# Optimization experiments

Hardware: AMD Instinct MI355X
Metric: run time of the kernel (lower is better)

## Reference

```python
import jax, jax.numpy as jnp
import numpy as np

TAU = 1.0       # softmax_temp
SOS_IDX = 1
EOS_IDX = 2
MAX_LEN = 20    # total message length incl. SOS/EOS -> 18 decode steps


def setup_inputs() -> dict:
    key = jax.random.key(0)
    ks = jax.random.split(key, 12)
    B, E, H, V, F = 512, 256, 512, 4096, 512
    T = MAX_LEN - 2
    s = lambda k, shape, sc: jax.random.normal(k, shape, jnp.float32) * sc
    return {
        "proto_a": s(ks[0], (B, F), 1.0),
        "proto_b": s(ks[1], (B, F), 1.0),
        "W_init": s(ks[2], (H, 2 * F), (2 * F) ** -0.5),
        "b_init": jnp.zeros((H,), jnp.float32),
        "W_ih": s(ks[3], (3 * H, E), E ** -0.5),
        "W_hh": s(ks[4], (3 * H, H), H ** -0.5),
        "b_ih": jnp.zeros((3 * H,), jnp.float32),
        "b_hh": jnp.zeros((3 * H,), jnp.float32),
        "W_out": s(ks[5], (V, H), H ** -0.5),
        "b_out": jnp.zeros((V,), jnp.float32),
        "emb": s(ks[6], (V, E), 1.0),
        # uniforms in (0,1) turned into Gumbel noise inside reference
        "u_gumbel": jax.random.uniform(ks[7], (T, B, V), jnp.float32, 1e-6, 1.0 - 1e-6),
    }


def reference(proto_a, proto_b, W_init, b_init, W_ih, W_hh, b_ih, b_hh,
              W_out, b_out, emb, u_gumbel):
    B = proto_a.shape[0]
    V = W_out.shape[0]
    # init_h(cat(prototypes, 1)) -> h0 [B, H]
    h0 = jnp.concatenate([proto_a, proto_b], axis=1) @ W_init.T + b_init
    sos = jnp.zeros((B, V), h0.dtype).at[:, SOS_IDX].set(1.0)
    eos = jnp.zeros((B, V), h0.dtype).at[:, EOS_IDX].set(1.0)
    x0 = sos @ emb  # [B, E]
    g = -jnp.log(-jnp.log(u_gumbel))  # Gumbel(0,1) noise, [T, B, V]

    def step(carry, gt):
        h, x = carry  # h [B,H], x [B,E]
        # PyTorch single-step GRU cell
        gi = x @ W_ih.T + b_ih
        gh = h @ W_hh.T + b_hh
        ir, iz, inn = jnp.split(gi, 3, axis=-1)
        hr, hz, hn = jnp.split(gh, 3, axis=-1)
        r = jax.nn.sigmoid(ir + hr)
        z = jax.nn.sigmoid(iz + hz)
        n = jnp.tanh(inn + r * hn)
        h_new = (1.0 - z) * n + z * h
        logits = h_new @ W_out.T + b_out  # [B, V]
        # gumbel_softmax(tau, hard=False) then straight-through hard one-hot
        y = jax.nn.softmax((logits + gt) / TAU, axis=-1)
        hard = jax.nn.one_hot(jnp.argmax(y, axis=-1), V, dtype=y.dtype)
        onehot = hard - jax.lax.stop_gradient(y) + y
        return (h_new, onehot @ emb), onehot

    _, toks = jax.lax.scan(step, (h0, x0), g)  # toks [T, B, V]
    lang = jnp.concatenate([sos[:, None], jnp.swapaxes(toks, 0, 1), eos[:, None]], axis=1)
    return lang  # [B, MAX_LEN, V]
```

## Files before the change

kernel.cpp:

```cpp
#include <hip/hip_runtime.h>
#include <hip/hip_bf16.h>
#include <math.h>

#define B_ 512
#define E_ 256
#define H_ 512
#define V_ 4096
#define T_ 18
#define L_ 20
#define MARGIN_ 0.04f
#define CCAP_ 64

typedef __attribute__((ext_vector_type(8))) short bf16x8;
typedef __attribute__((ext_vector_type(4))) float f32x4;

__global__ __launch_bounds__(256) void kprep32(const float* __restrict__ pa,
                                               const float* __restrict__ pb,
                                               const float* __restrict__ Wout,
                                               float* __restrict__ cat,
                                               __hip_bfloat16* __restrict__ WB) {
  int idx = blockIdx.x * 256 + threadIdx.x;
  if (idx < 131072) {
    int e0 = idx * 4;
    int b = e0 >> 10, k = e0 & 1023;
    float4 v = (k < 512) ? *reinterpret_cast<const float4*>(pa + (size_t)b * 512 + k)
                         : *reinterpret_cast<const float4*>(pb + (size_t)b * 512 + (k - 512));
    *reinterpret_cast<float4*>(cat + e0) = v;
  } else {
    int e0 = (idx - 131072) * 4;
    float4 w = *reinterpret_cast<const float4*>(Wout + e0);
    __hip_bfloat16 b0 = __float2bfloat16(w.x), b1 = __float2bfloat16(w.y);
    __hip_bfloat16 b2 = __float2bfloat16(w.z), b3 = __float2bfloat16(w.w);
    ushort4 o;
    o.x = *reinterpret_cast<unsigned short*>(&b0);
    o.y = *reinterpret_cast<unsigned short*>(&b1);
    o.z = *reinterpret_cast<unsigned short*>(&b2);
    o.w = *reinterpret_cast<unsigned short*>(&b3);
    *reinterpret_cast<ushort4*>(WB + e0) = o;
  }
}

__global__ __launch_bounds__(256) void sgemm128(const float* __restrict__ A,
                                                const float* __restrict__ W,
                                                float* __restrict__ P,
                                                int N, int lda, int kPer) {
  __shared__ float As[16][132];
  __shared__ float Bs[16][132];
  const int tid = threadIdx.x;
  const int tx = tid & 15, ty = tid >> 4;
  const int bn = blockIdx.x * 128, bm = blockIdx.y * 128;
  const int k0 = blockIdx.z * kPer;
  const size_t pOff = (size_t)blockIdx.z * (size_t)gridDim.y * 128 * N;
  const int r1 = tid >> 2;
  const int kq = (tid & 3) * 4;

  float acc[8][8] = {};
  for (int kb = 0; kb < kPer; kb += 16) {
    const float* Ap = A + (size_t)(bm + r1) * lda + k0 + kb + kq;
    const float* Wp = W + (size_t)(bn + r1) * lda + k0 + kb + kq;
    float4 a1 = *reinterpret_cast<const float4*>(Ap);
    float4 a2 = *reinterpret_cast<const float4*>(Ap + (size_t)64 * lda);
    float4 b1 = *reinterpret_cast<const float4*>(Wp);
    float4 b2 = *reinterpret_cast<const float4*>(Wp + (size_t)64 * lda);
    As[kq + 0][r1] = a1.x; As[kq + 1][r1] = a1.y;
    As[kq + 2][r1] = a1.z; As[kq + 3][r1] = a1.w;
    As[kq + 0][r1 + 64] = a2.x; As[kq + 1][r1 + 64] = a2.y;
    As[kq + 2][r1 + 64] = a2.z; As[kq + 3][r1 + 64] = a2.w;
    Bs[kq + 0][r1] = b1.x; Bs[kq + 1][r1] = b1.y;
    Bs[kq + 2][r1] = b1.z; Bs[kq + 3][r1] = b1.w;
    Bs[kq + 0][r1 + 64] = b2.x; Bs[kq + 1][r1 + 64] = b2.y;
    Bs[kq + 2][r1 + 64] = b2.z; Bs[kq + 3][r1 + 64] = b2.w;
    __syncthreads();
#pragma unroll
    for (int kk = 0; kk < 16; ++kk) {
      float a[8], b[8];
#pragma unroll
      for (int i = 0; i < 8; ++i) a[i] = As[kk][ty * 8 + i];
#pragma unroll
      for (int j = 0; j < 8; ++j) b[j] = Bs[kk][tx * 8 + j];
#pragma unroll
      for (int i = 0; i < 8; ++i)
#pragma unroll
        for (int j = 0; j < 8; ++j) acc[i][j] = fmaf(a[i], b[j], acc[i][j]);
    }
    __syncthreads();
  }
#pragma unroll
  for (int i = 0; i < 8; ++i) {
    size_t r = (size_t)(bm + ty * 8 + i);
    float4 v0 = make_float4(acc[i][0], acc[i][1], acc[i][2], acc[i][3]);
    float4 v1 = make_float4(acc[i][4], acc[i][5], acc[i][6], acc[i][7]);
    float4* dst = reinterpret_cast<float4*>(P + pOff + r * N + bn + tx * 8);
    dst[0] = v0;
    dst[1] = v1;
  }
}

__global__ __launch_bounds__(256) void reduceH0(const float* __restrict__ parts,
                                                const float* __restrict__ binit,
                                                float* __restrict__ h,
                                                __hip_bfloat16* __restrict__ hB) {
  int i = blockIdx.x * 256 + threadIdx.x;
  double s = (double)binit[i & 511];
#pragma unroll
  for (int c = 0; c < 8; ++c) s += (double)parts[(size_t)c * 262144 + i];
  float f = (float)s;
  h[i] = f;
  hB[i] = __float2bfloat16(f);
}

__device__ __forceinline__ void gh_gemm_body(const float* __restrict__ h,
                                             const float* __restrict__ Whh,
                                             float* __restrict__ ghP,
                                             int gid, int tid, char* smemRaw) {
  float (*As)[132] = reinterpret_cast<float(*)[132]>(smemRaw);
  float (*Bs)[132] = reinterpret_cast<float(*)[132]>(smemRaw + 8448);
  const int tx = tid & 15, ty = tid >> 4;
  const int bx = gid % 12, by = (gid / 12) & 3, bz = gid / 48;
  const int bn = bx * 128, bm = by * 128;
  const int k0 = bz * 64;
  const size_t pOff = (size_t)bz * 786432;
  const int r1 = tid >> 2, kq = (tid & 3) * 4;
  float acc[8][8] = {};
  for (int kb = 0; kb < 64; kb += 16) {
    const float* Ap = h   + (size_t)(bm + r1) * H_ + k0 + kb + kq;
    const float* Wp = Whh + (size_t)(bn + r1) * H_ + k0 + kb + kq;
    float4 a1 = *reinterpret_cast<const float4*>(Ap);
    float4 a2 = *reinterpret_cast<const float4*>(Ap + (size_t)64 * H_);
    float4 b1 = *reinterpret_cast<const float4*>(Wp);
    float4 b2 = *reinterpret_cast<const float4*>(Wp + (size_t)64 * H_);
    As[kq + 0][r1] = a1.x; As[kq + 1][r1] = a1.y;
    As[kq + 2][r1] = a1.z; As[kq + 3][r1] = a1.w;
    As[kq + 0][r1 + 64] = a2.x; As[kq + 1][r1 + 64] = a2.y;
    As[kq + 2][r1 + 64] = a2.z; As[kq + 3][r1 + 64] = a2.w;
    Bs[kq + 0][r1] = b1.x; Bs[kq + 1][r1] = b1.y;
    Bs[kq + 2][r1] = b1.z; Bs[kq + 3][r1] = b1.w;
    Bs[kq + 0][r1 + 64] = b2.x; Bs[kq + 1][r1 + 64] = b2.y;
    Bs[kq + 2][r1 + 64] = b2.z; Bs[kq + 3][r1 + 64] = b2.w;
    __syncthreads();
#pragma unroll
    for (int kk = 0; kk < 16; ++kk) {
      float a[8], b[8];
#pragma unroll
      for (int i = 0; i < 8; ++i) a[i] = As[kk][ty * 8 + i];
#pragma unroll
      for (int j = 0; j < 8; ++j) b[j] = Bs[kk][tx * 8 + j];
#pragma unroll
      for (int i = 0; i < 8; ++i)
#pragma unroll
        for (int j = 0; j < 8; ++j) acc[i][j] = fmaf(a[i], b[j], acc[i][j]);
    }
    __syncthreads();
  }
#pragma unroll
  for (int i = 0; i < 8; ++i) {
    size_t r = (size_t)(bm + ty * 8 + i);
    float4 v0 = make_float4(acc[i][0], acc[i][1], acc[i][2], acc[i][3]);
    float4 v1 = make_float4(acc[i][4], acc[i][5], acc[i][6], acc[i][7]);
    float4* dst = reinterpret_cast<float4*>(ghP + pOff + r * 1536 + bn + tx * 8);
    dst[0] = v0;
    dst[1] = v1;
  }
}

__device__ __forceinline__ void screen_body(const __hip_bfloat16* __restrict__ hB,
                                            const __hip_bfloat16* __restrict__ WoutB,
                                            float* __restrict__ loP,
                                            int bid, int tid) {
  const int wave = tid >> 6, lane = tid & 63;
  const int bx = bid & 63, by = bid >> 6;
  const int bm = by * 64 + wave * 16;
  const int bn = bx * 64;
  const int rA = lane & 15, g = lane >> 4;
  const __hip_bfloat16* ha = hB + (size_t)(bm + rA) * H_ + g * 8;
  const __hip_bfloat16* wb = WoutB + (size_t)(bn + rA) * H_ + g * 8;
  f32x4 acc[4] = {};
  for (int k0 = 0; k0 < H_; k0 += 32) {
    bf16x8 a = *reinterpret_cast<const bf16x8*>(ha + k0);
#pragma unroll
    for (int j = 0; j < 4; ++j) {
      bf16x8 b = *reinterpret_cast<const bf16x8*>(wb + (size_t)j * 16 * H_ + k0);
      acc[j] = __builtin_amdgcn_mfma_f32_16x16x32_bf16(a, b, acc[j], 0, 0, 0);
    }
  }
#pragma unroll
  for (int j = 0; j < 4; ++j)
#pragma unroll
    for (int r = 0; r < 4; ++r)
      loP[(size_t)(bm + g * 4 + r) * V_ + bn + j * 16 + rA] = acc[j][r];
}

__device__ __forceinline__ void gates_body(const float* __restrict__ ghP,
                                           const float* __restrict__ giP,
                                           const float* __restrict__ bih,
                                           const float* __restrict__ bhh,
                                           int tok, float* __restrict__ h,
                                           __hip_bfloat16* __restrict__ hB,
                                           int bid, int tid) {
  const float* g0 = giP + (size_t)tok * 1536;
  size_t base = (size_t)bid * 1536;
#pragma unroll
  for (int c = 0; c < 2; ++c) {
    int j = c * 256 + tid;
    int idx = bid * 512 + j;
    double gr = (double)bhh[j], gz = (double)bhh[512 + j], gn = (double)bhh[1024 + j];
#pragma unroll
    for (int s = 0; s < 8; ++s) {
      const float* p = ghP + (size_t)s * 786432 + base;
      gr += (double)p[j]; gz += (double)p[512 + j]; gn += (double)p[1024 + j];
    }
    float ir  = g0[j]        + bih[j];
    float iz  = g0[512 + j]  + bih[512 + j];
    float inn = g0[1024 + j] + bih[1024 + j];
    float r = 1.f / (1.f + expf(-(ir + (float)gr)));
    float z = 1.f / (1.f + expf(-(iz + (float)gz)));
    float n = tanhf(inn + r * (float)gn);
    float hn = (1.f - z) * n + z * h[idx];
    h[idx] = hn;
    hB[idx] = __float2bfloat16(hn);
  }
}

__device__ __forceinline__ int pick_body(const float* __restrict__ loP,
                                         const float* __restrict__ h,
                                         const float* __restrict__ Wout,
                                         const float* __restrict__ bout,
                                         const float* __restrict__ ub,
                                         int bid, int tid, char* smemRaw) {
  double* sd    = reinterpret_cast<double*>(smemRaw);
  int*    pre   = reinterpret_cast<int*>(smemRaw + 2048);
  int*    candV = reinterpret_cast<int*>(smemRaw + 3072);
  float*  swv   = reinterpret_cast<float*>(smemRaw + 3328);
  int*    swi   = reinterpret_cast<int*>(smemRaw + 3344);
  int*    sct   = reinterpret_cast<int*>(smemRaw + 3360);
  double* bestS = reinterpret_cast<double*>(smemRaw + 3376);
  int*    bestV = reinterpret_cast<int*>(smemRaw + 3384);
  const int lane = tid & 63, wv = tid >> 6;
  const float* l0 = loP + (size_t)bid * V_;
  float sloc[16];
  float best = -1e30f; int bi = 0x7fffffff;
#pragma unroll
  for (int i = 0; i < 16; ++i) {
    int v = tid + 256 * i;
    float s = l0[v] + bout[v] - logf(-logf(ub[v]));
    sloc[i] = s;
    if (s > best) { best = s; bi = v; }
  }
#pragma unroll
  for (int off = 1; off < 64; off <<= 1) {
    float ov = __shfl_xor(best, off, 64);
    int   oi = __shfl_xor(bi,  off, 64);
    if (ov > best || (ov == best && oi < bi)) { best = ov; bi = oi; }
  }
  if (lane == 0) { swv[wv] = best; swi[wv] = bi; }
  __syncthreads();
  float smax = swv[0]; int amax = swi[0];
#pragma unroll
  for (int w = 1; w < 4; ++w) {
    float ov = swv[w]; int oi = swi[w];
    if (ov > smax || (ov == smax && oi < amax)) { smax = ov; amax = oi; }
  }
  int c = 0;
#pragma unroll
  for (int i = 0; i < 16; ++i) if (sloc[i] >= smax - MARGIN_) ++c;
  int csum = c;
#pragma unroll
  for (int off = 1; off < 64; off <<= 1) csum += __shfl_xor(csum, off, 64);
  if (lane == 0) sct[wv] = csum;
  __syncthreads();
  int tot = sct[0] + sct[1] + sct[2] + sct[3];

  int tok;
  if (tot == 1) {
    tok = amax;
  } else if (tot <= CCAP_) {
    int lv[16];
    int cc = 0;
#pragma unroll
    for (int i = 0; i < 16; ++i)
      if (sloc[i] >= smax - MARGIN_) { if (cc < 16) lv[cc] = tid + 256 * i; ++cc; }
    pre[tid] = cc;
    __syncthreads();
    for (int off = 1; off < 256; off <<= 1) {
      int vv = (tid >= off) ? pre[tid - off] : 0;
      __syncthreads();
      pre[tid] += vv;
      __syncthreads();
    }
    int base = pre[tid] - cc;
    for (int q = 0; q < cc; ++q) candV[base + q] = lv[q];
    if (tid == 0) { *bestS = -1e300; *bestV = 0x7fffffff; }
    __syncthreads();
    const float* hb = h + (size_t)bid * H_;
    for (int ci = 0; ci < tot; ++ci) {
      int v = candV[ci];
      const float* wr = Wout + (size_t)v * H_;
      double p = (double)hb[tid] * (double)wr[tid]
               + (double)hb[tid + 256] * (double)wr[tid + 256];
#pragma unroll
      for (int off = 1; off < 64; off <<= 1) p += __shfl_xor(p, off, 64);
      if (lane == 0) sd[wv] = p;
      __syncthreads();
      if (tid == 0) {
        double s = sd[0] + sd[1] + sd[2] + sd[3]
                 + (double)bout[v] - log(-log((double)ub[v]));
        if (s > *bestS || (s == *bestS && v < *bestV)) { *bestS = s; *bestV = v; }
      }
      __syncthreads();
    }
    tok = *bestV;
  } else {
    const float* hb = h + (size_t)bid * H_;
    double dbest = -1e300; int dbi = 0x7fffffff;
    for (int i = 0; i < 16; ++i) {
      int v = tid + 256 * i;
      const float* wr = Wout + (size_t)v * H_;
      double dot = 0.0;
      for (int k = 0; k < H_; ++k) dot = fma((double)hb[k], (double)wr[k], dot);
      double s = dot + (double)bout[v] - log(-log((double)ub[v]));
      if (s > dbest) { dbest = s; dbi = v; }
    }
#pragma unroll
    for (int off = 1; off < 64; off <<= 1) {
      double od = __shfl_xor(dbest, off, 64);
      int    oi = __shfl_xor(dbi,  off, 64);
      if (od > dbest || (od == dbest && oi < dbi)) { dbest = od; dbi = oi; }
    }
    if (lane == 0) { sd[wv] = dbest; pre[wv] = dbi; }
    __syncthreads();
    double bs = sd[0]; int bv = pre[0];
#pragma unroll
    for (int w = 1; w < 4; ++w) {
      if (sd[w] > bs || (sd[w] == bs && pre[w] < bv)) { bs = sd[w]; bv = pre[w]; }
    }
    tok = bv;
  }
  return tok;
}

__global__ __launch_bounds__(256) void gates_init(const float* __restrict__ ghP,
                                                  const float* __restrict__ giP,
                                                  const float* __restrict__ bih,
                                                  const float* __restrict__ bhh,
                                                  float* __restrict__ h,
                                                  __hip_bfloat16* __restrict__ hB) {
  gates_body(ghP, giP, bih, bhh, 1, h, hB, blockIdx.x, threadIdx.x);
}

__global__ __launch_bounds__(256) void fusedA(const float* __restrict__ h,
                                              const float* __restrict__ Whh,
                                              const __hip_bfloat16* __restrict__ hB,
                                              const __hip_bfloat16* __restrict__ WoutB,
                                              float* __restrict__ ghP,
                                              float* __restrict__ loP,
                                              int doGemm) {
  __shared__ __align__(16) char smemRaw[16896];
  const int bid = blockIdx.x, tid = threadIdx.x;
  if (bid < 384) {
    if (doGemm) gh_gemm_body(h, Whh, ghP, bid, tid, smemRaw);
  } else {
    screen_body(hB, WoutB, loP, bid - 384, tid);
  }
}

__global__ __launch_bounds__(256) void fusedB(const float* __restrict__ loP,
                                              float* __restrict__ h,
                                              const float* __restrict__ Wout,
                                              const float* __restrict__ bout,
                                              const float* __restrict__ u,
                                              const float* __restrict__ ghP,
                                              const float* __restrict__ giP,
                                              const float* __restrict__ bih,
                                              const float* __restrict__ bhh,
                                              __hip_bfloat16* __restrict__ hB,
                                              int* __restrict__ toks,
                                              int t, int doGates) {
  __shared__ __align__(16) char smemRaw[5440];
  const int bid = blockIdx.x, tid = threadIdx.x;
  const int j0 = tid, j1 = 256 + tid;
  double gr0 = (double)bhh[j0], gz0 = (double)bhh[512 + j0], gn0 = (double)bhh[1024 + j0];
  double gr1 = (double)bhh[j1], gz1 = (double)bhh[512 + j1], gn1 = (double)bhh[1024 + j1];
  if (doGates) {
    size_t base = (size_t)bid * 1536;
#pragma unroll
    for (int s = 0; s < 8; ++s) {
      const float* p = ghP + (size_t)s * 786432 + base;
      gr0 += (double)p[j0]; gz0 += (double)p[512 + j0]; gn0 += (double)p[1024 + j0];
      gr1 += (double)p[j1]; gz1 += (double)p[512 + j1]; gn1 += (double)p[1024 + j1];
    }
  }
  const float* ub = u + (size_t)bid * V_;
  int tok = pick_body(loP, h, Wout, bout, ub, bid, tid, smemRaw);
  if (tid == 0) toks[t * B_ + bid] = tok;
  if (doGates) {
    const float* g0 = giP + (size_t)tok * 1536;
    {
      int idx = bid * 512 + j0;
      float ir  = g0[j0]        + bih[j0];
      float iz  = g0[512 + j0]  + bih[512 + j0];
      float inn = g0[1024 + j0] + bih[1024 + j0];
      float r = 1.f / (1.f + expf(-(ir + (float)gr0)));
      float z = 1.f / (1.f + expf(-(iz + (float)gz0)));
      float n = tanhf(inn + r * (float)gn0);
      float hn = (1.f - z) * n + z * h[idx];
      h[idx] = hn;
      hB[idx] = __float2bfloat16(hn);
    }
    {
      int idx = bid * 512 + j1;
      float ir  = g0[j1]        + bih[j1];
      float iz  = g0[512 + j1]  + bih[512 + j1];
      float inn = g0[1024 + j1] + bih[1024 + j1];
      float r = 1.f / (1.f + expf(-(ir + (float)gr1)));
      float z = 1.f / (1.f + expf(-(iz + (float)gz1)));
      float n = tanhf(inn + r * (float)gn1);
      float hn = (1.f - z) * n + z * h[idx];
      h[idx] = hn;
      hB[idx] = __float2bfloat16(hn);
    }
  }
}

__global__ __launch_bounds__(256) void kfinal32(float* __restrict__ out,
                                                const int* __restrict__ toks) {
  size_t c = (size_t)blockIdx.x * 256 + threadIdx.x;
  size_t e0 = c * 4;
  int v0 = (int)(e0 & (size_t)(V_ - 1));
  size_t row = e0 >> 12;
  int p = (int)(row % L_);
  int b = (int)(row / L_);
  int tok;
  if (p == 0)           tok = 1;
  else if (p == L_ - 1) tok = 2;
  else                  tok = toks[(p - 1) * B_ + b];
  float4 val = make_float4(0.f, 0.f, 0.f, 0.f);
  int d = tok - v0;
  if (d >= 0 && d < 4) {
    if (d == 0) val.x = 1.f; else if (d == 1) val.y = 1.f;
    else if (d == 2) val.z = 1.f; else val.w = 1.f;
  }
  reinterpret_cast<float4*>(out)[c] = val;
}

__global__ void kmark_ws(float* out) {
  if (threadIdx.x == 0) out[0] = 16.0f;
}
__global__ void kmark_resolver(float* out) {
  if (threadIdx.x == 0) out[2] = 11.0f;
}

extern "C" void kernel_launch(void* const* d_in, const int* in_sizes, int n_in,
                              void* d_out, int out_size, void* d_ws, size_t ws_size,
                              hipStream_t stream) {
  static const int EXPECT[12] = {262144, 262144, 524288, 512, 393216, 786432,
                                 1536, 1536, 2097152, 4096, 1048576, 37748736};
  const float* R[12];
  bool resolved = (n_in == 12);
  if (resolved) {
    bool used[12] = {};
    for (int i = 0; i < 12; ++i) {
      int f = -1;
      for (int j = 0; j < 12; ++j)
        if (!used[j] && in_sizes[j] == EXPECT[i]) { f = j; break; }
      if (f < 0) { resolved = false; break; }
      used[f] = true;
      R[i] = (const float*)d_in[f];
    }
  }
  if (!resolved)
    for (int i = 0; i < 12 && i < n_in; ++i) R[i] = (const float*)d_in[i];

  const float *pa = R[0], *pb = R[1], *Winit = R[2], *binit = R[3],
              *Wih = R[4], *Whh = R[5], *bih = R[6], *bhh = R[7],
              *Wout = R[8], *bout = R[9], *emb = R[10], *ug = R[11];
  float* out = (float*)d_out;

  const size_t TOK_BYTES = (size_t)T_ * B_ * sizeof(int);
  if (ws_size < TOK_BYTES) { kmark_ws<<<1, 64, 0, stream>>>(out); return; }
  int* toks = (int*)d_ws;

  const size_t SC_FLOATS = 16121856;
  float* sc;
  if (ws_size >= 40960 + SC_FLOATS * sizeof(float)) {
    sc = (float*)((char*)d_ws + 40960);
  } else {
    sc = (float*)d_out;
  }
  float* h    = sc;
  float* giP  = sc + 262144;
  float* ghP  = sc + 6553600;
  float* loP  = sc + 12845056;
  __hip_bfloat16* hB    = (__hip_bfloat16*)(sc + 14942208);
  __hip_bfloat16* WoutB = (__hip_bfloat16*)(sc + 15073280);
  float* cat  = ghP;
  float* h0P  = ghP + 524288;

  kprep32<<<2560, 256, 0, stream>>>(pa, pb, Wout, cat, WoutB);
  sgemm128<<<dim3(4, 4, 8), 256, 0, stream>>>(cat, Winit, h0P, 512, 1024, 128);
  reduceH0<<<1024, 256, 0, stream>>>(h0P, binit, h, hB);
  sgemm128<<<dim3(12, 32, 1), 256, 0, stream>>>(emb, Wih, giP, 1536, 256, 256);
  sgemm128<<<dim3(12, 4, 8), 256, 0, stream>>>(h, Whh, ghP, 1536, 512, 64);
  gates_init<<<512, 256, 0, stream>>>(ghP, giP, bih, bhh, h, hB);

  for (int t = 0; t < T_; ++t) {
    const float* uslice = ug + (size_t)t * B_ * V_;
    int notLast = (t < T_ - 1) ? 1 : 0;
    fusedA<<<896, 256, 0, stream>>>(h, Whh, hB, WoutB, ghP, loP, notLast);
    fusedB<<<512, 256, 0, stream>>>(loP, h, Wout, bout, uslice, ghP, giP,
                                    bih, bhh, hB, toks, t, notLast);
  }

  kfinal32<<<40960, 256, 0, stream>>>(out, toks);
  if (!resolved) kmark_resolver<<<1, 64, 0, stream>>>(out);
}
```

Before: 945.5 us.

## Fuse gumbel noise and bias into screen GEMM epilogue with per-block max pruning

Moves the bias add and Gumbel noise computation into the bf16 logit screening GEMM epilogue and records a per-64-column block maximum for each row. The pick kernel then reduces the 64 block maxima and scans only the blocks within the margin, instead of reading the full 4096-wide row plus noise on every step. This cuts the work and memory traffic in the serial pick stage. In exchange, the GEMM epilogue does the log computations and writes an extra bMax buffer, and the exact-rescore path now reloads the full row.

```diff
diff --git a/kernel.cpp b/kernel.cpp
--- a/kernel.cpp
+++ b/kernel.cpp
@@ -165,7 +165,10 @@
 
 __device__ __forceinline__ void screen_body(const __hip_bfloat16* __restrict__ hB,
                                             const __hip_bfloat16* __restrict__ WoutB,
+                                            const float* __restrict__ bout,
+                                            const float* __restrict__ u,
                                             float* __restrict__ loP,
+                                            float* __restrict__ bMax,
                                             int bid, int tid) {
   const int wave = tid >> 6, lane = tid & 63;
   const int bx = bid & 63, by = bid >> 6;
@@ -183,102 +186,97 @@
       acc[j] = __builtin_amdgcn_mfma_f32_16x16x32_bf16(a, b, acc[j], 0, 0, 0);
     }
   }
-#pragma unroll
-  for (int j = 0; j < 4; ++j)
-#pragma unroll
-    for (int r = 0; r < 4; ++r)
-      loP[(size_t)(bm + g * 4 + r) * V_ + bn + j * 16 + rA] = acc[j][r];
-}
-
-__device__ __forceinline__ void gates_body(const float* __restrict__ ghP,
-                                           const float* __restrict__ giP,
-                                           const float* __restrict__ bih,
-                                           const float* __restrict__ bhh,
-                                           int tok, float* __restrict__ h,
-                                           __hip_bfloat16* __restrict__ hB,
-                                           int bid, int tid) {
-  const float* g0 = giP + (size_t)tok * 1536;
-  size_t base = (size_t)bid * 1536;
-#pragma unroll
-  for (int c = 0; c < 2; ++c) {
-    int j = c * 256 + tid;
-    int idx = bid * 512 + j;
-    double gr = (double)bhh[j], gz = (double)bhh[512 + j], gn = (double)bhh[1024 + j];
-#pragma unroll
-    for (int s = 0; s < 8; ++s) {
-      const float* p = ghP + (size_t)s * 786432 + base;
-      gr += (double)p[j]; gz += (double)p[512 + j]; gn += (double)p[1024 + j];
-    }
-    float ir  = g0[j]        + bih[j];
-    float iz  = g0[512 + j]  + bih[512 + j];
-    float inn = g0[1024 + j] + bih[1024 + j];
-    float r = 1.f / (1.f + expf(-(ir + (float)gr)));
-    float z = 1.f / (1.f + expf(-(iz + (float)gz)));
-    float n = tanhf(inn + r * (float)gn);
-    float hn = (1.f - z) * n + z * h[idx];
-    h[idx] = hn;
-    hB[idx] = __float2bfloat16(hn);
+  float bj[4];
+#pragma unroll
+  for (int j = 0; j < 4; ++j) bj[j] = bout[bn + j * 16 + rA];
+#pragma unroll
+  for (int r = 0; r < 4; ++r) {
+    int row = bm + g * 4 + r;
+    const float* ur = u + (size_t)row * V_ + bn;
+    float m = -1e30f;
+#pragma unroll
+    for (int j = 0; j < 4; ++j) {
+      float s = acc[j][r] + bj[j] - logf(-logf(ur[j * 16 + rA]));
+      loP[(size_t)row * V_ + bn + j * 16 + rA] = s;
+      m = fmaxf(m, s);
+    }
+#pragma unroll
+    for (int off = 1; off < 16; off <<= 1) m = fmaxf(m, __shfl_xor(m, off, 64));
+    if (rA == 0) bMax[(size_t)row * 64 + bx] = m;
   }
 }
 
 __device__ __forceinline__ int pick_body(const float* __restrict__ loP,
+                                         const float* __restrict__ bMax,
                                          const float* __restrict__ h,
                                          const float* __restrict__ Wout,
                                          const float* __restrict__ bout,
                                          const float* __restrict__ ub,
                                          int bid, int tid, char* smemRaw) {
   double* sd    = reinterpret_cast<double*>(smemRaw);
-  int*    pre   = reinterpret_cast<int*>(smemRaw + 2048);
-  int*    candV = reinterpret_cast<int*>(smemRaw + 3072);
-  float*  swv   = reinterpret_cast<float*>(smemRaw + 3328);
-  int*    swi   = reinterpret_cast<int*>(smemRaw + 3344);
-  int*    sct   = reinterpret_cast<int*>(smemRaw + 3360);
-  double* bestS = reinterpret_cast<double*>(smemRaw + 3376);
-  int*    bestV = reinterpret_cast<int*>(smemRaw + 3384);
+  double* bestS = reinterpret_cast<double*>(smemRaw + 32);
+  int*    bestV = reinterpret_cast<int*>(smemRaw + 40);
+  int*    sNcb  = reinterpret_cast<int*>(smemRaw + 44);
+  float*  sRow  = reinterpret_cast<float*>(smemRaw + 48);
+  float*  swv   = reinterpret_cast<float*>(smemRaw + 56);
+  int*    swi   = reinterpret_cast<int*>(smemRaw + 72);
+  int*    sct   = reinterpret_cast<int*>(smemRaw + 88);
+  int*    candB = reinterpret_cast<int*>(smemRaw + 104);
+  int*    candV = reinterpret_cast<int*>(smemRaw + 360);
+  int*    pre   = reinterpret_cast<int*>(smemRaw + 640);
   const int lane = tid & 63, wv = tid >> 6;
   const float* l0 = loP + (size_t)bid * V_;
-  float sloc[16];
-  float best = -1e30f; int bi = 0x7fffffff;
-#pragma unroll
-  for (int i = 0; i < 16; ++i) {
-    int v = tid + 256 * i;
-    float s = l0[v] + bout[v] - logf(-logf(ub[v]));
-    sloc[i] = s;
-    if (s > best) { best = s; bi = v; }
+
+  if (wv == 0) {
+    float bm = bMax[(size_t)bid * 64 + lane];
+    float m = bm;
+#pragma unroll
+    for (int off = 1; off < 64; off <<= 1) m = fmaxf(m, __shfl_xor(m, off, 64));
+    unsigned long long mask = __ballot(bm >= m - MARGIN_);
+    int pos = __popcll(mask & ((1ull << lane) - 1ull));
+    if (bm >= m - MARGIN_) candB[pos] = lane;
+    if (lane == 0) { *sRow = m; *sNcb = __popcll(mask); }
+  }
+  __syncthreads();
+  float smax = *sRow;
+  int ncb = *sNcb;
+
+  float best = -1e30f; int bi = 0x7fffffff; int cnt = 0;
+  for (int e = tid; e < ncb * 64; e += 256) {
+    int v = candB[e >> 6] * 64 + (e & 63);
+    float s = l0[v];
+    if (s > best || (s == best && v < bi)) { best = s; bi = v; }
+    if (s >= smax - MARGIN_) ++cnt;
   }
 #pragma unroll
   for (int off = 1; off < 64; off <<= 1) {
     float ov = __shfl_xor(best, off, 64);
     int   oi = __shfl_xor(bi,  off, 64);
     if (ov > best || (ov == best && oi < bi)) { best = ov; bi = oi; }
-  }
-  if (lane == 0) { swv[wv] = best; swi[wv] = bi; }
+    cnt += __shfl_xor(cnt, off, 64);
+  }
+  if (lane == 0) { swv[wv] = best; swi[wv] = bi; sct[wv] = cnt; }
   __syncthreads();
-  float smax = swv[0]; int amax = swi[0];
+  float gmax = swv[0]; int amax = swi[0];
 #pragma unroll
   for (int w = 1; w < 4; ++w) {
     float ov = swv[w]; int oi = swi[w];
-    if (ov > smax || (ov == smax && oi < amax)) { smax = ov; amax = oi; }
-  }
-  int c = 0;
-#pragma unroll
-  for (int i = 0; i < 16; ++i) if (sloc[i] >= smax - MARGIN_) ++c;
-  int csum = c;
-#pragma unroll
-  for (int off = 1; off < 64; off <<= 1) csum += __shfl_xor(csum, off, 64);
-  if (lane == 0) sct[wv] = csum;
-  __syncthreads();
+    if (ov > gmax || (ov == gmax && oi < amax)) { gmax = ov; amax = oi; }
+  }
   int tot = sct[0] + sct[1] + sct[2] + sct[3];
 
   int tok;
   if (tot == 1) {
     tok = amax;
   } else if (tot <= CCAP_) {
+    float sloc[16];
+#pragma unroll
+    for (int i = 0; i < 16; ++i) sloc[i] = l0[tid + 256 * i];
     int lv[16];
     int cc = 0;
 #pragma unroll
     for (int i = 0; i < 16; ++i)
-      if (sloc[i] >= smax - MARGIN_) { if (cc < 16) lv[cc] = tid + 256 * i; ++cc; }
+      if (sloc[i] >= gmax - MARGIN_) { if (cc < 16) lv[cc] = tid + 256 * i; ++cc; }
     pre[tid] = cc;
     __syncthreads();
     for (int off = 1; off < 256; off <<= 1) {
@@ -344,26 +342,52 @@
                                                   const float* __restrict__ bhh,
                                                   float* __restrict__ h,
                                                   __hip_bfloat16* __restrict__ hB) {
-  gates_body(ghP, giP, bih, bhh, 1, h, hB, blockIdx.x, threadIdx.x);
+  const int bid = blockIdx.x, tid = threadIdx.x;
+  const float* g0 = giP + (size_t)1 * 1536;
+  size_t base = (size_t)bid * 1536;
+#pragma unroll
+  for (int c = 0; c < 2; ++c) {
+    int j = c * 256 + tid;
+    int idx = bid * 512 + j;
+    double gr = (double)bhh[j], gz = (double)bhh[512 + j], gn = (double)bhh[1024 + j];
+#pragma unroll
+    for (int s = 0; s < 8; ++s) {
+      const float* p = ghP + (size_t)s * 786432 + base;
+      gr += (double)p[j]; gz += (double)p[512 + j]; gn += (double)p[1024 + j];
+    }
+    float ir  = g0[j]        + bih[j];
+    float iz  = g0[512 + j]  + bih[512 + j];
+    float inn = g0[1024 + j] + bih[1024 + j];
+    float r = 1.f / (1.f + expf(-(ir + (float)gr)));
+    float z = 1.f / (1.f + expf(-(iz + (float)gz)));
+    float n = tanhf(inn + r * (float)gn);
+    float hn = (1.f - z) * n + z * h[idx];
+    h[idx] = hn;
+    hB[idx] = __float2bfloat16(hn);
+  }
 }
 
 __global__ __launch_bounds__(256) void fusedA(const float* __restrict__ h,
                                               const float* __restrict__ Whh,
                                               const __hip_bfloat16* __restrict__ hB,
                                               const __hip_bfloat16* __restrict__ WoutB,
+                                              const float* __restrict__ bout,
+                                              const float* __restrict__ u,
                                               float* __restrict__ ghP,
                                               float* __restrict__ loP,
+                                              float* __restrict__ bMax,
                                               int doGemm) {
   __shared__ __align__(16) char smemRaw[16896];
   const int bid = blockIdx.x, tid = threadIdx.x;
   if (bid < 384) {
     if (doGemm) gh_gemm_body(h, Whh, ghP, bid, tid, smemRaw);
   } else {
-    screen_body(hB, WoutB, loP, bid - 384, tid);
+    screen_body(hB, WoutB, bout, u, loP, bMax, bid - 384, tid);
   }
 }
 
 __global__ __launch_bounds__(256) void fusedB(const float* __restrict__ loP,
+                                              const float* __restrict__ bMax,
                                               float* __restrict__ h,
                                               const float* __restrict__ Wout,
                                               const float* __restrict__ bout,
@@ -375,7 +399,7 @@
                                               __hip_bfloat16* __restrict__ hB,
                                               int* __restrict__ toks,
                                               int t, int doGates) {
-  __shared__ __align__(16) char smemRaw[5440];
+  __shared__ __align__(16) char smemRaw[2048];
   const int bid = blockIdx.x, tid = threadIdx.x;
   const int j0 = tid, j1 = 256 + tid;
   double gr0 = (double)bhh[j0], gz0 = (double)bhh[512 + j0], gn0 = (double)bhh[1024 + j0];
@@ -390,7 +414,7 @@
     }
   }
   const float* ub = u + (size_t)bid * V_;
-  int tok = pick_body(loP, h, Wout, bout, ub, bid, tid, smemRaw);
+  int tok = pick_body(loP, bMax, h, Wout, bout, ub, bid, tid, smemRaw);
   if (tid == 0) toks[t * B_ + bid] = tok;
   if (doGates) {
     const float* g0 = giP + (size_t)tok * 1536;
@@ -479,7 +503,7 @@
   if (ws_size < TOK_BYTES) { kmark_ws<<<1, 64, 0, stream>>>(out); return; }
   int* toks = (int*)d_ws;
 
-  const size_t SC_FLOATS = 16121856;
+  const size_t SC_FLOATS = 16154624;
   float* sc;
   if (ws_size >= 40960 + SC_FLOATS * sizeof(float)) {
     sc = (float*)((char*)d_ws + 40960);
@@ -492,6 +516,7 @@
   float* loP  = sc + 12845056;
   __hip_bfloat16* hB    = (__hip_bfloat16*)(sc + 14942208);
   __hip_bfloat16* WoutB = (__hip_bfloat16*)(sc + 15073280);
+  float* bMax = sc + 16121856;
   float* cat  = ghP;
   float* h0P  = ghP + 524288;
 
@@ -505,8 +530,9 @@
   for (int t = 0; t < T_; ++t) {
     const float* uslice = ug + (size_t)t * B_ * V_;
     int notLast = (t < T_ - 1) ? 1 : 0;
-    fusedA<<<896, 256, 0, stream>>>(h, Whh, hB, WoutB, ghP, loP, notLast);
-    fusedB<<<512, 256, 0, stream>>>(loP, h, Wout, bout, uslice, ghP, giP,
+    fusedA<<<896, 256, 0, stream>>>(h, Whh, hB, WoutB, bout, uslice,
+                                    ghP, loP, bMax, notLast);
+    fusedB<<<512, 256, 0, stream>>>(loP, bMax, h, Wout, bout, uslice, ghP, giP,
                                     bih, bhh, hB, toks, t, notLast);
   }
 
```

Measured after the change: 1.016 ms. 7.5% more time.

## Shrink FP32 GEMM tiles to 128x64 and fuse setup GEMMs into one launch

Applied to the files above, without the earlier changes.

Replaces the 128x128-tile SGEMM with a 128x64-tile body that has a strided per-thread output mapping and scalar loads. Doubles block count for the per-step W_hh GEMM inside fusedA. Merges the W_init and W_ih setup GEMMs into a single launch. The aim is more parallelism and fewer launches, at the cost of less reuse per block, uncoalesced scalar global loads and scalar stores.

```diff
diff --git a/kernel.cpp b/kernel.cpp
--- a/kernel.cpp
+++ b/kernel.cpp
@@ -40,60 +40,79 @@
   }
 }
 
-__global__ __launch_bounds__(256) void sgemm128(const float* __restrict__ A,
-                                                const float* __restrict__ W,
-                                                float* __restrict__ P,
-                                                int N, int lda, int kPer) {
-  __shared__ float As[16][132];
-  __shared__ float Bs[16][132];
-  const int tid = threadIdx.x;
+__device__ __forceinline__ void gemm64_body(const float* __restrict__ A,
+                                            const float* __restrict__ W,
+                                            float* __restrict__ P,
+                                            int N, int lda, int kPer,
+                                            int bx, int by, int bz, int My,
+                                            int tid, char* smemRaw) {
+  float (*As)[130] = reinterpret_cast<float(*)[130]>(smemRaw);
+  float (*Bs)[68]  = reinterpret_cast<float(*)[68]>(smemRaw + 8320);
   const int tx = tid & 15, ty = tid >> 4;
-  const int bn = blockIdx.x * 128, bm = blockIdx.y * 128;
-  const int k0 = blockIdx.z * kPer;
-  const size_t pOff = (size_t)blockIdx.z * (size_t)gridDim.y * 128 * N;
-  const int r1 = tid >> 2;
-  const int kq = (tid & 3) * 4;
-
-  float acc[8][8] = {};
+  const int bn = bx * 64, bm = by * 128;
+  const int k0 = bz * kPer;
+  const size_t pOff = (size_t)bz * My * 128 * N;
+  const int kk0 = tid & 15;
+  const int ra0 = (tid >> 4) * 8;
+  const int cb0 = (tid >> 4) * 4;
+
+  float acc[8][4] = {};
   for (int kb = 0; kb < kPer; kb += 16) {
-    const float* Ap = A + (size_t)(bm + r1) * lda + k0 + kb + kq;
-    const float* Wp = W + (size_t)(bn + r1) * lda + k0 + kb + kq;
-    float4 a1 = *reinterpret_cast<const float4*>(Ap);
-    float4 a2 = *reinterpret_cast<const float4*>(Ap + (size_t)64 * lda);
-    float4 b1 = *reinterpret_cast<const float4*>(Wp);
-    float4 b2 = *reinterpret_cast<const float4*>(Wp + (size_t)64 * lda);
-    As[kq + 0][r1] = a1.x; As[kq + 1][r1] = a1.y;
-    As[kq + 2][r1] = a1.z; As[kq + 3][r1] = a1.w;
-    As[kq + 0][r1 + 64] = a2.x; As[kq + 1][r1 + 64] = a2.y;
-    As[kq + 2][r1 + 64] = a2.z; As[kq + 3][r1 + 64] = a2.w;
-    Bs[kq + 0][r1] = b1.x; Bs[kq + 1][r1] = b1.y;
-    Bs[kq + 2][r1] = b1.z; Bs[kq + 3][r1] = b1.w;
-    Bs[kq + 0][r1 + 64] = b2.x; Bs[kq + 1][r1 + 64] = b2.y;
-    Bs[kq + 2][r1 + 64] = b2.z; Bs[kq + 3][r1 + 64] = b2.w;
+#pragma unroll
+    for (int q = 0; q < 8; ++q)
+      As[kk0][ra0 + q] = A[(size_t)(bm + ra0 + q) * lda + k0 + kb + kk0];
+#pragma unroll
+    for (int q = 0; q < 4; ++q)
+      Bs[kk0][cb0 + q] = W[(size_t)(bn + cb0 + q) * lda + k0 + kb + kk0];
     __syncthreads();
 #pragma unroll
     for (int kk = 0; kk < 16; ++kk) {
-      float a[8], b[8];
-#pragma unroll
-      for (int i = 0; i < 8; ++i) a[i] = As[kk][ty * 8 + i];
-#pragma unroll
-      for (int j = 0; j < 8; ++j) b[j] = Bs[kk][tx * 8 + j];
+      float a[8], b[4];
+#pragma unroll
+      for (int i = 0; i < 8; ++i) a[i] = As[kk][ty + 16 * i];
+#pragma unroll
+      for (int j = 0; j < 4; ++j) b[j] = Bs[kk][tx + 16 * j];
 #pragma unroll
       for (int i = 0; i < 8; ++i)
 #pragma unroll
-        for (int j = 0; j < 8; ++j) acc[i][j] = fmaf(a[i], b[j], acc[i][j]);
+        for (int j = 0; j < 4; ++j) acc[i][j] = fmaf(a[i], b[j], acc[i][j]);
     }
     __syncthreads();
   }
 #pragma unroll
   for (int i = 0; i < 8; ++i) {
-    size_t r = (size_t)(bm + ty * 8 + i);
-    float4 v0 = make_float4(acc[i][0], acc[i][1], acc[i][2], acc[i][3]);
-    float4 v1 = make_float4(acc[i][4], acc[i][5], acc[i][6], acc[i][7]);
-    float4* dst = reinterpret_cast<float4*>(P + pOff + r * N + bn + tx * 8);
-    dst[0] = v0;
-    dst[1] = v1;
-  }
+    size_t r = (size_t)(bm + ty + 16 * i);
+#pragma unroll
+    for (int j = 0; j < 4; ++j)
+      P[pOff + r * N + bn + tx + 16 * j] = acc[i][j];
+  }
+}
+
+__global__ __launch_bounds__(256) void setupGemms(const float* __restrict__ cat,
+                                                  const float* __restrict__ Winit,
+                                                  float* __restrict__ h0P,
+                                                  const float* __restrict__ emb,
+                                                  const float* __restrict__ Wih,
+                                                  float* __restrict__ giP) {
+  __shared__ __align__(16) char smemRaw[12672];
+  const int bid = blockIdx.x, tid = threadIdx.x;
+  if (bid < 256) {
+    int bx = bid & 7, by = (bid >> 3) & 3, bz = bid >> 5;
+    gemm64_body(cat, Winit, h0P, 512, 1024, 128, bx, by, bz, 4, tid, smemRaw);
+  } else {
+    int gid = bid - 256;
+    int bx = gid % 24, by = gid / 24;
+    gemm64_body(emb, Wih, giP, 1536, 256, 256, bx, by, 0, 32, tid, smemRaw);
+  }
+}
+
+__global__ __launch_bounds__(256) void ghK(const float* __restrict__ h,
+                                           const float* __restrict__ Whh,
+                                           float* __restrict__ ghP) {
+  __shared__ __align__(16) char smemRaw[12672];
+  const int bid = blockIdx.x, tid = threadIdx.x;
+  int bx = bid % 24, by = (bid / 24) & 3, bz = bid / 96;
+  gemm64_body(h, Whh, ghP, 1536, 512, 64, bx, by, bz, 4, tid, smemRaw);
 }
 
 __global__ __launch_bounds__(256) void reduceH0(const float* __restrict__ parts,
@@ -107,60 +126,6 @@
   float f = (float)s;
   h[i] = f;
   hB[i] = __float2bfloat16(f);
-}
-
-__device__ __forceinline__ void gh_gemm_body(const float* __restrict__ h,
-                                             const float* __restrict__ Whh,
-                                             float* __restrict__ ghP,
-                                             int gid, int tid, char* smemRaw) {
-  float (*As)[132] = reinterpret_cast<float(*)[132]>(smemRaw);
-  float (*Bs)[132] = reinterpret_cast<float(*)[132]>(smemRaw + 8448);
-  const int tx = tid & 15, ty = tid >> 4;
-  const int bx = gid % 12, by = (gid / 12) & 3, bz = gid / 48;
-  const int bn = bx * 128, bm = by * 128;
-  const int k0 = bz * 64;
-  const size_t pOff = (size_t)bz * 786432;
-  const int r1 = tid >> 2, kq = (tid & 3) * 4;
-  float acc[8][8] = {};
-  for (int kb = 0; kb < 64; kb += 16) {
-    const float* Ap = h   + (size_t)(bm + r1) * H_ + k0 + kb + kq;
-    const float* Wp = Whh + (size_t)(bn + r1) * H_ + k0 + kb + kq;
-    float4 a1 = *reinterpret_cast<const float4*>(Ap);
-    float4 a2 = *reinterpret_cast<const float4*>(Ap + (size_t)64 * H_);
-    float4 b1 = *reinterpret_cast<const float4*>(Wp);
-    float4 b2 = *reinterpret_cast<const float4*>(Wp + (size_t)64 * H_);
-    As[kq + 0][r1] = a1.x; As[kq + 1][r1] = a1.y;
-    As[kq + 2][r1] = a1.z; As[kq + 3][r1] = a1.w;
-    As[kq + 0][r1 + 64] = a2.x; As[kq + 1][r1 + 64] = a2.y;
-    As[kq + 2][r1 + 64] = a2.z; As[kq + 3][r1 + 64] = a2.w;
-    Bs[kq + 0][r1] = b1.x; Bs[kq + 1][r1] = b1.y;
-    Bs[kq + 2][r1] = b1.z; Bs[kq + 3][r1] = b1.w;
-    Bs[kq + 0][r1 + 64] = b2.x; Bs[kq + 1][r1 + 64] = b2.y;
-    Bs[kq + 2][r1 + 64] = b2.z; Bs[kq + 3][r1 + 64] = b2.w;
-    __syncthreads();
-#pragma unroll
-    for (int kk = 0; kk < 16; ++kk) {
-      float a[8], b[8];
-#pragma unroll
-      for (int i = 0; i < 8; ++i) a[i] = As[kk][ty * 8 + i];
-#pragma unroll
-      for (int j = 0; j < 8; ++j) b[j] = Bs[kk][tx * 8 + j];
-#pragma unroll
-      for (int i = 0; i < 8; ++i)
-#pragma unroll
-        for (int j = 0; j < 8; ++j) acc[i][j] = fmaf(a[i], b[j], acc[i][j]);
-    }
-    __syncthreads();
-  }
-#pragma unroll
-  for (int i = 0; i < 8; ++i) {
-    size_t r = (size_t)(bm + ty * 8 + i);
-    float4 v0 = make_float4(acc[i][0], acc[i][1], acc[i][2], acc[i][3]);
-    float4 v1 = make_float4(acc[i][4], acc[i][5], acc[i][6], acc[i][7]);
-    float4* dst = reinterpret_cast<float4*>(ghP + pOff + r * 1536 + bn + tx * 8);
-    dst[0] = v0;
-    dst[1] = v1;
-  }
 }
 
 __device__ __forceinline__ void screen_body(const __hip_bfloat16* __restrict__ hB,
@@ -188,37 +153,6 @@
 #pragma unroll
     for (int r = 0; r < 4; ++r)
       loP[(size_t)(bm + g * 4 + r) * V_ + bn + j * 16 + rA] = acc[j][r];
-}
-
-__device__ __forceinline__ void gates_body(const float* __restrict__ ghP,
-                                           const float* __restrict__ giP,
-                                           const float* __restrict__ bih,
-                                           const float* __restrict__ bhh,
-                                           int tok, float* __restrict__ h,
-                                           __hip_bfloat16* __restrict__ hB,
-                                           int bid, int tid) {
-  const float* g0 = giP + (size_t)tok * 1536;
-  size_t base = (size_t)bid * 1536;
-#pragma unroll
-  for (int c = 0; c < 2; ++c) {
-    int j = c * 256 + tid;
-    int idx = bid * 512 + j;
-    double gr = (double)bhh[j], gz = (double)bhh[512 + j], gn = (double)bhh[1024 + j];
-#pragma unroll
-    for (int s = 0; s < 8; ++s) {
-      const float* p = ghP + (size_t)s * 786432 + base;
-      gr += (double)p[j]; gz += (double)p[512 + j]; gn += (double)p[1024 + j];
-    }
-    float ir  = g0[j]        + bih[j];
-    float iz  = g0[512 + j]  + bih[512 + j];
-    float inn = g0[1024 + j] + bih[1024 + j];
-    float r = 1.f / (1.f + expf(-(ir + (float)gr)));
-    float z = 1.f / (1.f + expf(-(iz + (float)gz)));
-    float n = tanhf(inn + r * (float)gn);
-    float hn = (1.f - z) * n + z * h[idx];
-    h[idx] = hn;
-    hB[idx] = __float2bfloat16(hn);
-  }
 }
 
 __device__ __forceinline__ int pick_body(const float* __restrict__ loP,
@@ -344,7 +278,29 @@
                                                   const float* __restrict__ bhh,
                                                   float* __restrict__ h,
                                                   __hip_bfloat16* __restrict__ hB) {
-  gates_body(ghP, giP, bih, bhh, 1, h, hB, blockIdx.x, threadIdx.x);
+  const int bid = blockIdx.x, tid = threadIdx.x;
+  const float* g0 = giP + (size_t)1 * 1536;
+  size_t base = (size_t)bid * 1536;
+#pragma unroll
+  for (int c = 0; c < 2; ++c) {
+    int j = c * 256 + tid;
+    int idx = bid * 512 + j;
+    double gr = (double)bhh[j], gz = (double)bhh[512 + j], gn = (double)bhh[1024 + j];
+#pragma unroll
+    for (int s = 0; s < 8; ++s) {
+      const float* p = ghP + (size_t)s * 786432 + base;
+      gr += (double)p[j]; gz += (double)p[512 + j]; gn += (double)p[1024 + j];
+    }
+    float ir  = g0[j]        + bih[j];
+    float iz  = g0[512 + j]  + bih[512 + j];
+    float inn = g0[1024 + j] + bih[1024 + j];
+    float r = 1.f / (1.f + expf(-(ir + (float)gr)));
+    float z = 1.f / (1.f + expf(-(iz + (float)gz)));
+    float n = tanhf(inn + r * (float)gn);
+    float hn = (1.f - z) * n + z * h[idx];
+    h[idx] = hn;
+    hB[idx] = __float2bfloat16(hn);
+  }
 }
 
 __global__ __launch_bounds__(256) void fusedA(const float* __restrict__ h,
@@ -354,12 +310,15 @@
                                               float* __restrict__ ghP,
                                               float* __restrict__ loP,
                                               int doGemm) {
-  __shared__ __align__(16) char smemRaw[16896];
+  __shared__ __align__(16) char smemRaw[12672];
   const int bid = blockIdx.x, tid = threadIdx.x;
-  if (bid < 384) {
-    if (doGemm) gh_gemm_body(h, Whh, ghP, bid, tid, smemRaw);
+  if (bid < 768) {
+    if (doGemm) {
+      int bx = bid % 24, by = (bid / 24) & 3, bz = bid / 96;
+      gemm64_body(h, Whh, ghP, 1536, 512, 64, bx, by, bz, 4, tid, smemRaw);
+    }
   } else {
-    screen_body(hB, WoutB, loP, bid - 384, tid);
+    screen_body(hB, WoutB, loP, bid - 768, tid);
   }
 }
 
@@ -496,16 +455,15 @@
   float* h0P  = ghP + 524288;
 
   kprep32<<<2560, 256, 0, stream>>>(pa, pb, Wout, cat, WoutB);
-  sgemm128<<<dim3(4, 4, 8), 256, 0, stream>>>(cat, Winit, h0P, 512, 1024, 128);
+  setupGemms<<<1024, 256, 0, stream>>>(cat, Winit, h0P, emb, Wih, giP);
   reduceH0<<<1024, 256, 0, stream>>>(h0P, binit, h, hB);
-  sgemm128<<<dim3(12, 32, 1), 256, 0, stream>>>(emb, Wih, giP, 1536, 256, 256);
-  sgemm128<<<dim3(12, 4, 8), 256, 0, stream>>>(h, Whh, ghP, 1536, 512, 64);
+  ghK<<<768, 256, 0, stream>>>(h, Whh, ghP);
   gates_init<<<512, 256, 0, stream>>>(ghP, giP, bih, bhh, h, hB);
 
   for (int t = 0; t < T_; ++t) {
     const float* uslice = ug + (size_t)t * B_ * V_;
     int notLast = (t < T_ - 1) ? 1 : 0;
-    fusedA<<<896, 256, 0, stream>>>(h, Whh, hB, WoutB, ghP, loP, notLast);
+    fusedA<<<1280, 256, 0, stream>>>(h, Whh, hB, WoutB, ghP, loP, notLast);
     fusedB<<<512, 256, 0, stream>>>(loP, h, Wout, bout, uslice, ghP, giP,
                                     bih, bhh, hB, toks, t, notLast);
   }
```

New measurement: 917.6 us. -2.9%, faster.
